# Kernel optimization log

Hardware: AMD Instinct MI355X
Metric: run time of the kernel (lower is better)

## Reference

```python
import jax, jax.numpy as jnp
import numpy as np

B, S, D = 2, 2048, 4096
H, KVH, HD = 32, 8, 128
WIN = 1024  # sliding window
THETA = 10000.0


def setup_inputs() -> dict:
    key = jax.random.key(0)
    ks = jax.random.split(key, 5)
    x = jax.random.normal(ks[0], (B, S, D), jnp.float32) * 0.02
    wq = jax.random.normal(ks[1], (H * HD, D), jnp.float32) * 0.02
    wk = jax.random.normal(ks[2], (KVH * HD, D), jnp.float32) * 0.02
    wv = jax.random.normal(ks[3], (KVH * HD, D), jnp.float32) * 0.02
    wo = jax.random.normal(ks[4], (D, H * HD), jnp.float32) * 0.02
    positions = jnp.arange(S, dtype=jnp.int32)
    inv_freq = 1.0 / (THETA ** (jnp.arange(0, HD, 2, dtype=jnp.float32) / HD))
    ang = positions.astype(jnp.float32)[:, None] * inv_freq[None, :]  # [S, HD/2]
    cos, sin = jnp.cos(ang), jnp.sin(ang)
    i = jnp.arange(S)[:, None]
    j = jnp.arange(S)[None, :]
    allowed = (j <= i) & (i - j < WIN)  # causal + sliding window
    mask = jnp.where(allowed, 0.0, -1e9).astype(jnp.float32)  # [S, S]
    return {"x": x, "wq": wq, "wk": wk, "wv": wv, "wo": wo,
            "cos": cos, "sin": sin, "mask": mask, "positions": positions}


def _apply_rope(t, cos, sin):
    # t: [B, S, nH, HD]; pairs are consecutive dims (torch view_as_complex layout)
    tr = t.reshape(t.shape[:-1] + (HD // 2, 2))
    t0, t1 = tr[..., 0], tr[..., 1]
    c = cos[None, :, None, :]
    s = sin[None, :, None, :]
    out = jnp.stack([t0 * c - t1 * s, t0 * s + t1 * c], axis=-1)
    return out.reshape(t.shape)


def reference(x, wq, wk, wv, wo, cos, sin, mask, positions):
    bsz, seqlen, _ = x.shape
    xq = (x @ wq.T).reshape(bsz, seqlen, H, HD)
    xk = (x @ wk.T).reshape(bsz, seqlen, KVH, HD)
    xv = (x @ wv.T).reshape(bsz, seqlen, KVH, HD)
    xq = _apply_rope(xq, cos, sin)
    xk = _apply_rope(xk, cos, sin)
    # GQA: repeat_kv head broadcast (prefill path: positions.size(0) > 1)
    rep = H // KVH
    key = jnp.repeat(xk, rep, axis=2)  # [B, S, H, HD]
    val = jnp.repeat(xv, rep, axis=2)
    q = xq.transpose(0, 2, 1, 3)  # [B, H, S, HD]
    k = key.transpose(0, 2, 1, 3)
    v = val.transpose(0, 2, 1, 3)
    scale = HD ** -0.5
    scores = jnp.einsum("bhqd,bhkd->bhqk", q, k) * scale
    scores = scores + mask[None, None, :, :]
    probs = jax.nn.softmax(scores.astype(jnp.float32), axis=-1).astype(q.dtype)
    out = jnp.einsum("bhqk,bhkd->bhqd", probs, v)
    out = out.transpose(0, 2, 1, 3).reshape(bsz, seqlen, H * HD)
    return out @ wo.T
```

## Files before the change

kernel.cpp:

```cpp
#include <hip/hip_runtime.h>
#include <hip/hip_bf16.h>

#define B_  2
#define S_  2048
#define D_  4096
#define H_  32
#define KVH_ 8
#define HD_ 128
#define WIN_ 1024
#define KVSTR 2048

typedef __attribute__((ext_vector_type(8))) __bf16 bf16x8;
typedef __attribute__((ext_vector_type(4))) float f32x4;
using bf16 = __hip_bfloat16;

typedef const __attribute__((address_space(1))) void* gas_ptr;
typedef __attribute__((address_space(3))) void* las_ptr;

__device__ __forceinline__ void gload16(const void* g, void* l) {
    __builtin_amdgcn_global_load_lds((gas_ptr)g, (las_ptr)l, 16, 0, 0);
}

__device__ __forceinline__ bf16x8 load8(const bf16* p) {
    return *reinterpret_cast<const bf16x8*>(p);
}
__device__ __forceinline__ bf16x8 cvt8(const bf16* p) {
    return *reinterpret_cast<const bf16x8*>(p);
}
__device__ __forceinline__ bf16x8 cvt8(const float* p) {
    const float4* q = reinterpret_cast<const float4*>(p);
    float4 a = q[0], b = q[1];
    bf16x8 r;
    r[0] = (__bf16)a.x; r[1] = (__bf16)a.y; r[2] = (__bf16)a.z; r[3] = (__bf16)a.w;
    r[4] = (__bf16)b.x; r[5] = (__bf16)b.y; r[6] = (__bf16)b.z; r[7] = (__bf16)b.w;
    return r;
}
__device__ __forceinline__ void store1(float* p, float v) { *p = v; }
__device__ __forceinline__ void store1(bf16* p, float v) { *p = __float2bfloat16(v); }

#define GBAR()  __builtin_amdgcn_s_barrier()
#define SCB0()  __builtin_amdgcn_sched_barrier(0)
#define LGKM0() do { asm volatile("s_waitcnt lgkmcnt(0)" ::: "memory"); \
                     __builtin_amdgcn_sched_barrier(0); } while (0)
#define VMC(n)  do { asm volatile("s_waitcnt vmcnt(" #n ")" ::: "memory"); \
                     __builtin_amdgcn_sched_barrier(0); } while (0)

__global__ __launch_bounds__(256) void cast_kernel(const float* __restrict__ in,
                                                   bf16* __restrict__ out) {
    long i = ((long)blockIdx.x * 256 + threadIdx.x) * 8;
    const float4* p = reinterpret_cast<const float4*>(in + i);
    float4 a = p[0], b = p[1];
    bf16x8 r;
    r[0] = (__bf16)a.x; r[1] = (__bf16)a.y; r[2] = (__bf16)a.z; r[3] = (__bf16)a.w;
    r[4] = (__bf16)b.x; r[5] = (__bf16)b.y; r[6] = (__bf16)b.z; r[7] = (__bf16)b.w;
    *reinterpret_cast<bf16x8*>(out + i) = r;
}

__global__ __launch_bounds__(256) void cast2_kernel(
    const float* __restrict__ in0, bf16* __restrict__ out0,
    const float* __restrict__ in1, bf16* __restrict__ out1, int n0blocks) {
    const bool first = (int)blockIdx.x < n0blocks;
    const float* in = first ? in0 : in1;
    bf16* out = first ? out0 : out1;
    long bid = first ? blockIdx.x : (blockIdx.x - n0blocks);
    long i = (bid * 256 + threadIdx.x) * 8;
    const float4* p = reinterpret_cast<const float4*>(in + i);
    float4 a = p[0], b = p[1];
    bf16x8 r;
    r[0] = (__bf16)a.x; r[1] = (__bf16)a.y; r[2] = (__bf16)a.z; r[3] = (__bf16)a.w;
    r[4] = (__bf16)b.x; r[5] = (__bf16)b.y; r[6] = (__bf16)b.z; r[7] = (__bf16)b.w;
    *reinterpret_cast<bf16x8*>(out + i) = r;
}

__device__ __forceinline__ void xcd_swizzle(int& bx, int& by, int nbx, int nby) {
    int flat = bx + nbx * by;
    int nwg  = nbx * nby;
    int cpx  = nwg >> 3;
    int swz  = (flat & 7) * cpx + (flat >> 3);
    bx = swz % nbx;
    by = swz / nbx;
}

template <typename TC>
__global__ __launch_bounds__(512, 2) void gemm_nt_256(
    const bf16* __restrict__ A, const bf16* __restrict__ Bm,
    TC* __restrict__ C, int M, int N, int K) {
    __shared__ __bf16 lds[2][2][256 * 64];

    const int tid  = threadIdx.x;
    const int wave = tid >> 6;
    const int lane = tid & 63;
    const int col  = lane & 15;
    const int quad = lane >> 4;
    const int c7   = col & 7;
    const int wmi  = wave >> 2;
    const int wni  = wave & 3;
    int bx = blockIdx.x, by = blockIdx.y;
    xcd_swizzle(bx, by, gridDim.x, gridDim.y);
    const long m0  = (long)by * 256;
    const long n0  = (long)bx * 256;
    const int  nt  = K >> 6;

    f32x4 zero = {0.f, 0.f, 0.f, 0.f};
    f32x4 acc[8][4];
#pragma unroll
    for (int i = 0; i < 8; i++)
#pragma unroll
        for (int j = 0; j < 4; j++) acc[i][j] = zero;

    long gA[4], gB[4];
    int  lofs[4];
#pragma unroll
    for (int j = 0; j < 4; j++) {
        int r  = j * 64 + wave * 8 + (lane >> 3);
        int cg = (lane & 7) ^ (r & 7);
        gA[j]   = (m0 + r) * (long)K + cg * 8;
        gB[j]   = (n0 + r) * (long)K + cg * 8;
        lofs[j] = (j * 64 + wave * 8) * 128;
    }

#pragma unroll
    for (int j = 0; j < 4; j++) {
        gload16(A  + gA[j], (char*)lds[0][0] + lofs[j]);
        gload16(Bm + gB[j], (char*)lds[0][1] + lofs[j]);
    }
    if (nt > 1) {
#pragma unroll
        for (int j = 0; j < 4; j++)
            gload16(Bm + gB[j] + 64, (char*)lds[1][1] + lofs[j]);
        gload16(A + gA[0] + 64, (char*)lds[1][0] + lofs[0]);
        gload16(A + gA[2] + 64, (char*)lds[1][0] + lofs[2]);
        VMC(6);
    } else {
        VMC(0);
    }
    GBAR();

#define RDA_(dst, mf, ks) \
    dst = *reinterpret_cast<const bf16x8*>(Ab + (wmi * 128 + (mf) * 16 + col) * 128 \
                                              + ((((ks) << 2) + quad) ^ c7) * 16)
#define MFMA16(mb) \
    do { \
        _Pragma("unroll") \
        for (int ks = 0; ks < 2; ks++) { \
            _Pragma("unroll") \
            for (int nf = 0; nf < 4; nf++) { \
                acc[mb][nf]     = __builtin_amdgcn_mfma_f32_16x16x32_bf16( \
                    a[0][ks], bfr[nf][ks], acc[mb][nf], 0, 0, 0); \
                acc[mb + 1][nf] = __builtin_amdgcn_mfma_f32_16x16x32_bf16( \
                    a[1][ks], bfr[nf][ks], acc[mb + 1][nf], 0, 0, 0); \
            } \
        } \
    } while (0)

    for (int t = 0; t < nt; ++t) {
        const int cur = t & 1;
        const char* Ab = (const char*)lds[cur][0];
        const char* Bb = (const char*)lds[cur][1];
        char* An2 = (char*)lds[cur ^ 1][0];
        char* Ac2 = (char*)lds[cur][0];
        char* Bc2 = (char*)lds[cur][1];

        bf16x8 bfr[4][2];
#pragma unroll
        for (int nf = 0; nf < 4; nf++)
#pragma unroll
            for (int ks = 0; ks < 2; ks++)
                bfr[nf][ks] = *reinterpret_cast<const bf16x8*>(
                    Bb + (wni * 64 + nf * 16 + col) * 128 + (((ks << 2) + quad) ^ c7) * 16);
        bf16x8 a[2][2];
        RDA_(a[0][0], 0, 0); RDA_(a[0][1], 0, 1);
        RDA_(a[1][0], 1, 0); RDA_(a[1][1], 1, 1);
        if (t + 1 < nt) {
            long ko = (long)(t + 1) * 64;
            gload16(A + gA[1] + ko, An2 + lofs[1]);
            gload16(A + gA[3] + ko, An2 + lofs[3]);
        }
        GBAR();
        LGKM0();
        __builtin_amdgcn_s_setprio(1);
        MFMA16(0);
        __builtin_amdgcn_s_setprio(0);
        GBAR();

        RDA_(a[0][0], 2, 0); RDA_(a[0][1], 2, 1);
        RDA_(a[1][0], 3, 0); RDA_(a[1][1], 3, 1);
        if (t + 2 < nt) {
            long ko = (long)(t + 2) * 64;
#pragma unroll
            for (int j = 0; j < 4; j++)
                gload16(Bm + gB[j] + ko, Bc2 + lofs[j]);
        }
        GBAR();
        LGKM0();
        __builtin_amdgcn_s_setprio(1);
        MFMA16(2);
        __builtin_amdgcn_s_setprio(0);
        GBAR();

        RDA_(a[0][0], 4, 0); RDA_(a[0][1], 4, 1);
        RDA_(a[1][0], 5, 0); RDA_(a[1][1], 5, 1);
        if (t + 2 < nt) {
            long ko = (long)(t + 2) * 64;
            gload16(A + gA[0] + ko, Ac2 + lofs[0]);
            gload16(A + gA[2] + ko, Ac2 + lofs[2]);
        }
        GBAR();
        LGKM0();
        __builtin_amdgcn_s_setprio(1);
        MFMA16(4);
        __builtin_amdgcn_s_setprio(0);
        GBAR();

        RDA_(a[0][0], 6, 0); RDA_(a[0][1], 6, 1);
        RDA_(a[1][0], 7, 0); RDA_(a[1][1], 7, 1);
        LGKM0();
        __builtin_amdgcn_s_setprio(1);
        MFMA16(6);
        __builtin_amdgcn_s_setprio(0);
        if (t + 2 < nt) { VMC(6); } else { VMC(0); }
        GBAR();
    }

#pragma unroll
    for (int mf = 0; mf < 8; mf++) {
#pragma unroll
        for (int nf = 0; nf < 4; nf++) {
            long row = m0 + wmi * 128 + mf * 16 + quad * 4;
            long cc  = n0 + wni * 64 + nf * 16 + col;
#pragma unroll
            for (int r = 0; r < 4; r++)
                store1(&C[(row + r) * (long)N + cc], acc[mf][nf][r]);
        }
    }
}

template <typename TC>
__global__ __launch_bounds__(256) void gemm_nt_fast(
    const bf16* __restrict__ A, const bf16* __restrict__ Bm,
    TC* __restrict__ C, int M, int N, int K) {
    __shared__ __bf16 As[128 * 64];
    __shared__ __bf16 Bs[128 * 64];

    const int tid  = threadIdx.x;
    const int wave = tid >> 6;
    const int lane = tid & 63;
    const int col  = lane & 15;
    const int quad = lane >> 4;
    const int c7   = col & 7;
    const int wm   = (wave >> 1) * 64;
    const int wn   = (wave & 1) * 64;
    int bx = blockIdx.x, by = blockIdx.y;
    xcd_swizzle(bx, by, gridDim.x, gridDim.y);
    const long m0  = (long)by * 128;
    const long n0  = (long)bx * 128;

    f32x4 zero = {0.f, 0.f, 0.f, 0.f};
    f32x4 acc[4][4];
#pragma unroll
    for (int i = 0; i < 4; i++)
#pragma unroll
        for (int j = 0; j < 4; j++) acc[i][j] = zero;

    long goffA[4], goffB[4];
    int  loff[4];
#pragma unroll
    for (int i = 0; i < 4; i++) {
        int r  = (wave * 4 + i) * 8 + (lane >> 3);
        int cg = (lane & 7) ^ (r & 7);
        goffA[i] = (m0 + r) * (long)K + cg * 8;
        goffB[i] = (n0 + r) * (long)K + cg * 8;
        loff[i]  = (wave * 4 + i) * 1024;
    }

    for (int kt = 0; kt < K; kt += 64) {
#pragma unroll
        for (int i = 0; i < 4; i++) {
            gload16(A + goffA[i] + kt, (char*)As + loff[i]);
            gload16(Bm + goffB[i] + kt, (char*)Bs + loff[i]);
        }
        __syncthreads();

        bf16x8 af[2][4], bfv[2][4];
#pragma unroll
        for (int ks = 0; ks < 2; ks++) {
#pragma unroll
            for (int mt = 0; mt < 4; mt++) {
                int row = wm + mt * 16 + col;
                af[ks][mt] = *reinterpret_cast<const bf16x8*>(
                    (const char*)As + row * 128 + (((ks << 2) + quad) ^ c7) * 16);
            }
#pragma unroll
            for (int nt = 0; nt < 4; nt++) {
                int row = wn + nt * 16 + col;
                bfv[ks][nt] = *reinterpret_cast<const bf16x8*>(
                    (const char*)Bs + row * 128 + (((ks << 2) + quad) ^ c7) * 16);
            }
        }
#pragma unroll
        for (int ks = 0; ks < 2; ks++)
#pragma unroll
            for (int mt = 0; mt < 4; mt++)
#pragma unroll
                for (int nt = 0; nt < 4; nt++)
                    acc[mt][nt] = __builtin_amdgcn_mfma_f32_16x16x32_bf16(
                        af[ks][mt], bfv[ks][nt], acc[mt][nt], 0, 0, 0);
        __syncthreads();
    }

#pragma unroll
    for (int mt = 0; mt < 4; mt++) {
#pragma unroll
        for (int nt = 0; nt < 4; nt++) {
            long row = m0 + wm + mt * 16 + quad * 4;
            long cc  = n0 + wn + nt * 16 + col;
#pragma unroll
            for (int r = 0; r < 4; r++)
                store1(&C[(row + r) * (long)N + cc], acc[mt][nt][r]);
        }
    }
}

template <typename TA, typename TB, typename TC>
__global__ __launch_bounds__(256) void gemm_nt(
    const TA* __restrict__ A, const TB* __restrict__ Bm,
    TC* __restrict__ C, int M, int N, int K, int ldc) {
    __shared__ __bf16 As[128 * 40];
    __shared__ __bf16 Bs[128 * 40];

    const int tid  = threadIdx.x;
    const int wave = tid >> 6;
    const int lane = tid & 63;
    const int col  = lane & 15;
    const int quad = lane >> 4;
    const int wm   = (wave >> 1) * 64;
    const int wn   = (wave & 1) * 64;
    const long m0  = (long)blockIdx.y * 128;
    const long n0  = (long)blockIdx.x * 128;

    f32x4 zero = {0.f, 0.f, 0.f, 0.f};
    f32x4 acc[4][4];
#pragma unroll
    for (int i = 0; i < 4; i++)
#pragma unroll
        for (int j = 0; j < 4; j++) acc[i][j] = zero;

    const int srow = tid >> 2;
    const int sch  = (tid & 3) * 8;

    for (int kt = 0; kt < K; kt += 32) {
        bf16x8 av0 = cvt8(A + (m0 + srow)      * (long)K + kt + sch);
        bf16x8 av1 = cvt8(A + (m0 + srow + 64) * (long)K + kt + sch);
        bf16x8 bv0 = cvt8(Bm + (n0 + srow)      * (long)K + kt + sch);
        bf16x8 bv1 = cvt8(Bm + (n0 + srow + 64) * (long)K + kt + sch);
        *reinterpret_cast<bf16x8*>(&As[srow * 40 + sch])        = av0;
        *reinterpret_cast<bf16x8*>(&As[(srow + 64) * 40 + sch]) = av1;
        *reinterpret_cast<bf16x8*>(&Bs[srow * 40 + sch])        = bv0;
        *reinterpret_cast<bf16x8*>(&Bs[(srow + 64) * 40 + sch]) = bv1;
        __syncthreads();

        bf16x8 af[4], bfv[4];
#pragma unroll
        for (int mt = 0; mt < 4; mt++)
            af[mt] = *reinterpret_cast<const bf16x8*>(&As[(wm + mt * 16 + col) * 40 + quad * 8]);
#pragma unroll
        for (int nt = 0; nt < 4; nt++)
            bfv[nt] = *reinterpret_cast<const bf16x8*>(&Bs[(wn + nt * 16 + col) * 40 + quad * 8]);
#pragma unroll
        for (int mt = 0; mt < 4; mt++)
#pragma unroll
            for (int nt = 0; nt < 4; nt++)
                acc[mt][nt] = __builtin_amdgcn_mfma_f32_16x16x32_bf16(
                    af[mt], bfv[nt], acc[mt][nt], 0, 0, 0);
        __syncthreads();
    }

#pragma unroll
    for (int mt = 0; mt < 4; mt++) {
#pragma unroll
        for (int nt = 0; nt < 4; nt++) {
            long row = m0 + wm + mt * 16 + quad * 4;
            long cc  = n0 + wn + nt * 16 + col;
#pragma unroll
            for (int r = 0; r < 4; r++)
                store1(&C[(row + r) * (long)ldc + cc], acc[mt][nt][r]);
        }
    }
}

__global__ __launch_bounds__(256) void rope_kv_kernel(
    bf16* __restrict__ kvb,
    const float* __restrict__ cosb, const float* __restrict__ sinb) {
    int idx = blockIdx.x * 256 + threadIdx.x;
    int pair = idx & 63;
    int rest = idx >> 6;
    int hh   = rest % KVH_;
    int tok  = rest / KVH_;
    int s    = tok & (S_ - 1);
    long base = (long)tok * KVSTR + hh * HD_ + pair * 2;
    float c  = cosb[s * 64 + pair];
    float sn = sinb[s * 64 + pair];
    float t0 = __bfloat162float(kvb[base]);
    float t1 = __bfloat162float(kvb[base + 1]);
    kvb[base]     = __float2bfloat16(t0 * c - t1 * sn);
    kvb[base + 1] = __float2bfloat16(t0 * sn + t1 * c);
}

__global__ __launch_bounds__(256) void transpose_v(const bf16* __restrict__ kv,
                                                   bf16* __restrict__ vt) {
    __shared__ __bf16 tile[64][72];
    const int s0 = blockIdx.x * 64;
    const int d0 = blockIdx.y * 64;
    const int b  = blockIdx.z;
    const int tid = threadIdx.x;
    const int tr  = tid >> 3;
    const int c8  = (tid & 7) * 8;
#pragma unroll
    for (int p = 0; p < 2; p++) {
        int srow = tr + p * 32;
        bf16x8 val = load8(kv + ((long)(b * S_ + s0 + srow)) * KVSTR + 1024 + d0 + c8);
        *reinterpret_cast<bf16x8*>(&tile[srow][c8]) = val;
    }
    __syncthreads();
#pragma unroll
    for (int p = 0; p < 2; p++) {
        int dd = tr + p * 32;
        bf16x8 ov;
#pragma unroll
        for (int j = 0; j < 8; j++) ov[j] = tile[c8 + j][dd];
        *reinterpret_cast<bf16x8*>(vt + ((long)(b * 1024 + d0 + dd)) * S_ + s0 + c8) = ov;
    }
}

__global__ __launch_bounds__(512, 4) void attn_kernel(
    const bf16* __restrict__ q, const bf16* __restrict__ kv,
    const bf16* __restrict__ vt, bf16* __restrict__ o,
    const float* __restrict__ cosb, const float* __restrict__ sinb) {
    const int qb  = blockIdx.x;
    const int hp  = blockIdx.y;
    const int b   = blockIdx.z;
    const int tid = threadIdx.x;
    const int wave = tid >> 6;
    const int lane = tid & 63;
    const int col  = lane & 15;
    const int quad = lane >> 4;
    const int h    = hp * 2 + (wave >> 2);
    const int wq4  = wave & 3;
    const int kvh  = hp >> 1;
    const int i0   = qb * 64;
    const float scale = 0.08838834764831845f;

    __shared__ __bf16 Ks[64 * 128];
    __shared__ __bf16 Vs[128 * 64];
    __shared__ __bf16 Pl[8][16 * 72];

    const int srow = i0 + wq4 * 16 + col;
    bf16x8 qa[4];
    {
        const bf16* qptr = q + ((long)(b * S_ + srow)) * (H_ * HD_) + h * HD_ + quad * 8;
#pragma unroll
        for (int ks = 0; ks < 4; ks++) {
            bf16x8 v = load8(qptr + ks * 32);
            float4 c4 = *reinterpret_cast<const float4*>(
                cosb + (long)srow * 64 + quad * 4 + ks * 16);
            float4 s4 = *reinterpret_cast<const float4*>(
                sinb + (long)srow * 64 + quad * 4 + ks * 16);
            bf16x8 r;
            float t0, t1;
            t0 = (float)v[0]; t1 = (float)v[1];
            r[0] = (__bf16)(t0 * c4.x - t1 * s4.x); r[1] = (__bf16)(t0 * s4.x + t1 * c4.x);
            t0 = (float)v[2]; t1 = (float)v[3];
            r[2] = (__bf16)(t0 * c4.y - t1 * s4.y); r[3] = (__bf16)(t0 * s4.y + t1 * c4.y);
            t0 = (float)v[4]; t1 = (float)v[5];
            r[4] = (__bf16)(t0 * c4.z - t1 * s4.z); r[5] = (__bf16)(t0 * s4.z + t1 * c4.z);
            t0 = (float)v[6]; t1 = (float)v[7];
            r[6] = (__bf16)(t0 * c4.w - t1 * s4.w); r[7] = (__bf16)(t0 * s4.w + t1 * c4.w);
            qa[ks] = r;
        }
    }

    long gK[2], gV[2];
    int  lK[2], lV[2];
#pragma unroll
    for (int i = 0; i < 2; i++) {
        int ck  = wave * 2 + i;
        int rK  = ck * 4 + (lane >> 4);
        int cgK = (lane & 15) ^ (rK & 15);
        gK[i] = ((long)(b * S_) + rK) * KVSTR + kvh * HD_ + cgK * 8;
        lK[i] = ck * 1024;
        int rV  = ck * 8 + (lane >> 3);
        int cgV = (lane & 7) ^ (rV & 7);
        gV[i] = ((long)(b * 1024) + kvh * HD_ + rV) * (long)S_ + cgV * 8;
        lV[i] = ck * 1024;
    }

    f32x4 zero = {0.f, 0.f, 0.f, 0.f};
    f32x4 oacc[8];
#pragma unroll
    for (int i = 0; i < 8; i++) oacc[i] = zero;
    float lsum[4] = {0.f, 0.f, 0.f, 0.f};

    const int kb0 = (qb >= 16) ? (qb - 16) : 0;

    bf16x8 kreg[2], vreg[2];
#pragma unroll
    for (int i = 0; i < 2; i++) {
        kreg[i] = *reinterpret_cast<const bf16x8*>(kv + gK[i] + (long)kb0 * 64 * KVSTR);
        vreg[i] = *reinterpret_cast<const bf16x8*>(vt + gV[i] + kb0 * 64);
    }

    for (int kb = kb0; kb <= qb; kb++) {
        GBAR();
        SCB0();
#pragma unroll
        for (int i = 0; i < 2; i++) {
            *reinterpret_cast<bf16x8*>((char*)Ks + lK[i] + lane * 16) = kreg[i];
            *reinterpret_cast<bf16x8*>((char*)Vs + lV[i] + lane * 16) = vreg[i];
        }
        LGKM0();
        GBAR();
        SCB0();
        if (kb < qb) {
#pragma unroll
            for (int i = 0; i < 2; i++) {
                kreg[i] = *reinterpret_cast<const bf16x8*>(
                    kv + gK[i] + (long)(kb + 1) * 64 * KVSTR);
                vreg[i] = *reinterpret_cast<const bf16x8*>(
                    vt + gV[i] + (kb + 1) * 64);
            }
            SCB0();
        }

        f32x4 sfr[4];
        __builtin_amdgcn_s_setprio(1);
#pragma unroll
        for (int nt = 0; nt < 4; nt++) {
            f32x4 s = zero;
            int row = nt * 16 + col;
#pragma unroll
            for (int ks = 0; ks < 4; ks++) {
                bf16x8 bfv = *reinterpret_cast<const bf16x8*>(
                    (const char*)Ks + row * 256 + (((ks << 2) + quad) ^ col) * 16);
                s = __builtin_amdgcn_mfma_f32_16x16x32_bf16(qa[ks], bfv, s, 0, 0, 0);
            }
            sfr[nt] = s;
        }
        __builtin_amdgcn_s_setprio(0);
#pragma unroll
        for (int nt = 0; nt < 4; nt++) {
            int j = kb * 64 + nt * 16 + col;
#pragma unroll
            for (int r = 0; r < 4; r++) {
                int i = i0 + wq4 * 16 + quad * 4 + r;
                float p = 0.f;
                if (j <= i && (i - j) < WIN_) p = __expf(sfr[nt][r] * scale);
                lsum[r] += p;
                Pl[wave][(quad * 4 + r) * 72 + nt * 16 + col] = __float2bfloat16(p);
            }
        }
        __builtin_amdgcn_s_setprio(1);
#pragma unroll
        for (int ks2 = 0; ks2 < 2; ks2++) {
            bf16x8 pa = *reinterpret_cast<const bf16x8*>(
                &Pl[wave][col * 72 + ks2 * 32 + quad * 8]);
#pragma unroll
            for (int nt2 = 0; nt2 < 8; nt2++) {
                int d = nt2 * 16 + col;
                bf16x8 vb = *reinterpret_cast<const bf16x8*>(
                    (const char*)Vs + d * 128 + ((((ks2 << 2) + quad)) ^ (col & 7)) * 16);
                oacc[nt2] = __builtin_amdgcn_mfma_f32_16x16x32_bf16(
                    pa, vb, oacc[nt2], 0, 0, 0);
            }
        }
        __builtin_amdgcn_s_setprio(0);
    }

#pragma unroll
    for (int m = 1; m < 16; m <<= 1) {
#pragma unroll
        for (int r = 0; r < 4; r++) lsum[r] += __shfl_xor(lsum[r], m, 64);
    }

    bf16* op = o + ((long)(b * S_ + i0 + wq4 * 16 + quad * 4)) * (H_ * HD_) + h * HD_;
#pragma unroll
    for (int nt2 = 0; nt2 < 8; nt2++) {
#pragma unroll
        for (int r = 0; r < 4; r++)
            op[(long)r * (H_ * HD_) + nt2 * 16 + col] =
                __float2bfloat16(oacc[nt2][r] / lsum[r]);
    }
}

extern "C" void kernel_launch(void* const* d_in, const int* in_sizes, int n_in,
                              void* d_out, int out_size, void* d_ws, size_t ws_size,
                              hipStream_t stream) {
    const float* x    = (const float*)d_in[0];
    const float* wq   = (const float*)d_in[1];
    const float* wk   = (const float*)d_in[2];
    const float* wv   = (const float*)d_in[3];
    const float* wo   = (const float*)d_in[4];
    const float* cosb = (const float*)d_in[5];
    const float* sinb = (const float*)d_in[6];
    float* out = (float*)d_out;

    const size_t T   = (size_t)B_ * S_;
    const size_t SZ_D  = T * (H_ * HD_);
    const size_t SZ_KV = T * (KVH_ * HD_);

    dim3 blk(256);
    const size_t need_fast = (SZ_D * 3 + SZ_KV * 3 + SZ_D) * 2;

    if (ws_size >= need_fast) {
        bf16* xb    = (bf16*)d_ws;
        bf16* wbuf  = xb    + SZ_D;
        bf16* q_ws  = wbuf  + SZ_D;
        bf16* kv_ws = q_ws  + SZ_D;
        bf16* vt_ws = kv_ws + 2 * SZ_KV;
        bf16* ao_ws = vt_ws + SZ_KV;

        cast2_kernel<<<2 * (SZ_D / 2048), blk, 0, stream>>>(x, xb, wq, wbuf,
                                                            (int)(SZ_D / 2048));
        gemm_nt_256<bf16><<<dim3(16, 16), dim3(512), 0, stream>>>(xb, wbuf, q_ws, 4096, 4096, 4096);

        cast2_kernel<<<2 * (SZ_KV / 2048), blk, 0, stream>>>(wk, wbuf, wv, wbuf + SZ_KV,
                                                             (int)(SZ_KV / 2048));
        gemm_nt_fast<bf16><<<dim3(16, 32), blk, 0, stream>>>(xb, wbuf, kv_ws, 4096, 2048, 4096);

        rope_kv_kernel<<<(B_ * S_ * KVH_ * 64) / 256, blk, 0, stream>>>(
            kv_ws, cosb, sinb);
        transpose_v<<<dim3(32, 16, 2), blk, 0, stream>>>(kv_ws, vt_ws);

        attn_kernel<<<dim3(32, 16, 2), dim3(512), 0, stream>>>(
            q_ws, kv_ws, vt_ws, ao_ws, cosb, sinb);

        cast_kernel<<<SZ_D / 2048, blk, 0, stream>>>(wo, wbuf);
        gemm_nt_256<float><<<dim3(16, 16), dim3(512), 0, stream>>>(ao_ws, wbuf, out, 4096, 4096, 4096);
    } else {
        bf16* q_ws  = (bf16*)d_ws;
        bf16* kv_ws = q_ws  + SZ_D;
        bf16* vt_ws = kv_ws + 2 * SZ_KV;
        bf16* ao_ws = vt_ws + SZ_KV;

        gemm_nt<float, float, bf16><<<dim3(32, 32), blk, 0, stream>>>(x, wq, q_ws, 4096, 4096, 4096, 4096);
        gemm_nt<float, float, bf16><<<dim3(8, 32),  blk, 0, stream>>>(x, wk, kv_ws, 4096, 1024, 4096, KVSTR);
        gemm_nt<float, float, bf16><<<dim3(8, 32),  blk, 0, stream>>>(x, wv, kv_ws + 1024, 4096, 1024, 4096, KVSTR);

        rope_kv_kernel<<<(B_ * S_ * KVH_ * 64) / 256, blk, 0, stream>>>(
            kv_ws, cosb, sinb);
        transpose_v<<<dim3(32, 16, 2), blk, 0, stream>>>(kv_ws, vt_ws);

        attn_kernel<<<dim3(32, 16, 2), dim3(512), 0, stream>>>(
            q_ws, kv_ws, vt_ws, ao_ws, cosb, sinb);

        gemm_nt<bf16, float, float><<<dim3(32, 32), blk, 0, stream>>>(ao_ws, wo, out, 4096, 4096, 4096, 4096);
    }
}
```

Before: 660.2 us.

## Fuse Q, K, V projections into one GEMM over a concatenated weight matrix

Concatenates wq, wk and wv into one bf16 weight buffer and runs a single 256-tile GEMM that writes an interleaved QKV buffer with row stride 6144. The RoPE, V-transpose and attention kernels are re-pointed at offsets inside that buffer. This removes the separate smaller KV GEMM and its tail, so the 384-block launch fills the GPU better. The attention output now reuses the x cast buffer to save workspace. The wider row stride can change cache and locality behaviour for the K loads in attention.

Result: slower. 707.5 us (+7.2%).

```diff
diff --git a/kernel.cpp b/kernel.cpp
--- a/kernel.cpp
+++ b/kernel.cpp
@@ -8,7 +8,9 @@
 #define KVH_ 8
 #define HD_ 128
 #define WIN_ 1024
-#define KVSTR 2048
+#define QKVSTR 6144
+#define KOFF   4096
+#define VOFF   5120
 
 typedef __attribute__((ext_vector_type(8))) __bf16 bf16x8;
 typedef __attribute__((ext_vector_type(4))) float f32x4;
@@ -235,92 +237,6 @@
     }
 }
 
-template <typename TC>
-__global__ __launch_bounds__(256) void gemm_nt_fast(
-    const bf16* __restrict__ A, const bf16* __restrict__ Bm,
-    TC* __restrict__ C, int M, int N, int K) {
-    __shared__ __bf16 As[128 * 64];
-    __shared__ __bf16 Bs[128 * 64];
-
-    const int tid  = threadIdx.x;
-    const int wave = tid >> 6;
-    const int lane = tid & 63;
-    const int col  = lane & 15;
-    const int quad = lane >> 4;
-    const int c7   = col & 7;
-    const int wm   = (wave >> 1) * 64;
-    const int wn   = (wave & 1) * 64;
-    int bx = blockIdx.x, by = blockIdx.y;
-    xcd_swizzle(bx, by, gridDim.x, gridDim.y);
-    const long m0  = (long)by * 128;
-    const long n0  = (long)bx * 128;
-
-    f32x4 zero = {0.f, 0.f, 0.f, 0.f};
-    f32x4 acc[4][4];
-#pragma unroll
-    for (int i = 0; i < 4; i++)
-#pragma unroll
-        for (int j = 0; j < 4; j++) acc[i][j] = zero;
-
-    long goffA[4], goffB[4];
-    int  loff[4];
-#pragma unroll
-    for (int i = 0; i < 4; i++) {
-        int r  = (wave * 4 + i) * 8 + (lane >> 3);
-        int cg = (lane & 7) ^ (r & 7);
-        goffA[i] = (m0 + r) * (long)K + cg * 8;
-        goffB[i] = (n0 + r) * (long)K + cg * 8;
-        loff[i]  = (wave * 4 + i) * 1024;
-    }
-
-    for (int kt = 0; kt < K; kt += 64) {
-#pragma unroll
-        for (int i = 0; i < 4; i++) {
-            gload16(A + goffA[i] + kt, (char*)As + loff[i]);
-            gload16(Bm + goffB[i] + kt, (char*)Bs + loff[i]);
-        }
-        __syncthreads();
-
-        bf16x8 af[2][4], bfv[2][4];
-#pragma unroll
-        for (int ks = 0; ks < 2; ks++) {
-#pragma unroll
-            for (int mt = 0; mt < 4; mt++) {
-                int row = wm + mt * 16 + col;
-                af[ks][mt] = *reinterpret_cast<const bf16x8*>(
-                    (const char*)As + row * 128 + (((ks << 2) + quad) ^ c7) * 16);
-            }
-#pragma unroll
-            for (int nt = 0; nt < 4; nt++) {
-                int row = wn + nt * 16 + col;
-                bfv[ks][nt] = *reinterpret_cast<const bf16x8*>(
-                    (const char*)Bs + row * 128 + (((ks << 2) + quad) ^ c7) * 16);
-            }
-        }
-#pragma unroll
-        for (int ks = 0; ks < 2; ks++)
-#pragma unroll
-            for (int mt = 0; mt < 4; mt++)
-#pragma unroll
-                for (int nt = 0; nt < 4; nt++)
-                    acc[mt][nt] = __builtin_amdgcn_mfma_f32_16x16x32_bf16(
-                        af[ks][mt], bfv[ks][nt], acc[mt][nt], 0, 0, 0);
-        __syncthreads();
-    }
-
-#pragma unroll
-    for (int mt = 0; mt < 4; mt++) {
-#pragma unroll
-        for (int nt = 0; nt < 4; nt++) {
-            long row = m0 + wm + mt * 16 + quad * 4;
-            long cc  = n0 + wn + nt * 16 + col;
-#pragma unroll
-            for (int r = 0; r < 4; r++)
-                store1(&C[(row + r) * (long)N + cc], acc[mt][nt][r]);
-        }
-    }
-}
-
 template <typename TA, typename TB, typename TC>
 __global__ __launch_bounds__(256) void gemm_nt(
     const TA* __restrict__ A, const TB* __restrict__ Bm,
@@ -389,7 +305,7 @@
 }
 
 __global__ __launch_bounds__(256) void rope_kv_kernel(
-    bf16* __restrict__ kvb,
+    bf16* __restrict__ qkv,
     const float* __restrict__ cosb, const float* __restrict__ sinb) {
     int idx = blockIdx.x * 256 + threadIdx.x;
     int pair = idx & 63;
@@ -397,16 +313,16 @@
     int hh   = rest % KVH_;
     int tok  = rest / KVH_;
     int s    = tok & (S_ - 1);
-    long base = (long)tok * KVSTR + hh * HD_ + pair * 2;
+    long base = (long)tok * QKVSTR + KOFF + hh * HD_ + pair * 2;
     float c  = cosb[s * 64 + pair];
     float sn = sinb[s * 64 + pair];
-    float t0 = __bfloat162float(kvb[base]);
-    float t1 = __bfloat162float(kvb[base + 1]);
-    kvb[base]     = __float2bfloat16(t0 * c - t1 * sn);
-    kvb[base + 1] = __float2bfloat16(t0 * sn + t1 * c);
-}
-
-__global__ __launch_bounds__(256) void transpose_v(const bf16* __restrict__ kv,
+    float t0 = __bfloat162float(qkv[base]);
+    float t1 = __bfloat162float(qkv[base + 1]);
+    qkv[base]     = __float2bfloat16(t0 * c - t1 * sn);
+    qkv[base + 1] = __float2bfloat16(t0 * sn + t1 * c);
+}
+
+__global__ __launch_bounds__(256) void transpose_v(const bf16* __restrict__ qkv,
                                                    bf16* __restrict__ vt) {
     __shared__ __bf16 tile[64][72];
     const int s0 = blockIdx.x * 64;
@@ -418,7 +334,7 @@
 #pragma unroll
     for (int p = 0; p < 2; p++) {
         int srow = tr + p * 32;
-        bf16x8 val = load8(kv + ((long)(b * S_ + s0 + srow)) * KVSTR + 1024 + d0 + c8);
+        bf16x8 val = load8(qkv + ((long)(b * S_ + s0 + srow)) * QKVSTR + VOFF + d0 + c8);
         *reinterpret_cast<bf16x8*>(&tile[srow][c8]) = val;
     }
     __syncthreads();
@@ -433,8 +349,8 @@
 }
 
 __global__ __launch_bounds__(512, 4) void attn_kernel(
-    const bf16* __restrict__ q, const bf16* __restrict__ kv,
-    const bf16* __restrict__ vt, bf16* __restrict__ o,
+    const bf16* __restrict__ qkv, const bf16* __restrict__ vt,
+    bf16* __restrict__ o,
     const float* __restrict__ cosb, const float* __restrict__ sinb) {
     const int qb  = blockIdx.x;
     const int hp  = blockIdx.y;
@@ -457,7 +373,7 @@
     const int srow = i0 + wq4 * 16 + col;
     bf16x8 qa[4];
     {
-        const bf16* qptr = q + ((long)(b * S_ + srow)) * (H_ * HD_) + h * HD_ + quad * 8;
+        const bf16* qptr = qkv + ((long)(b * S_ + srow)) * QKVSTR + h * HD_ + quad * 8;
 #pragma unroll
         for (int ks = 0; ks < 4; ks++) {
             bf16x8 v = load8(qptr + ks * 32);
@@ -486,7 +402,7 @@
         int ck  = wave * 2 + i;
         int rK  = ck * 4 + (lane >> 4);
         int cgK = (lane & 15) ^ (rK & 15);
-        gK[i] = ((long)(b * S_) + rK) * KVSTR + kvh * HD_ + cgK * 8;
+        gK[i] = ((long)(b * S_) + rK) * QKVSTR + KOFF + kvh * HD_ + cgK * 8;
         lK[i] = ck * 1024;
         int rV  = ck * 8 + (lane >> 3);
         int cgV = (lane & 7) ^ (rV & 7);
@@ -505,7 +421,7 @@
     bf16x8 kreg[2], vreg[2];
 #pragma unroll
     for (int i = 0; i < 2; i++) {
-        kreg[i] = *reinterpret_cast<const bf16x8*>(kv + gK[i] + (long)kb0 * 64 * KVSTR);
+        kreg[i] = *reinterpret_cast<const bf16x8*>(qkv + gK[i] + (long)kb0 * 64 * QKVSTR);
         vreg[i] = *reinterpret_cast<const bf16x8*>(vt + gV[i] + kb0 * 64);
     }
 
@@ -524,7 +440,7 @@
 #pragma unroll
             for (int i = 0; i < 2; i++) {
                 kreg[i] = *reinterpret_cast<const bf16x8*>(
-                    kv + gK[i] + (long)(kb + 1) * 64 * KVSTR);
+                    qkv + gK[i] + (long)(kb + 1) * 64 * QKVSTR);
                 vreg[i] = *reinterpret_cast<const bf16x8*>(
                     vt + gV[i] + (kb + 1) * 64);
             }
@@ -603,55 +519,60 @@
     const float* sinb = (const float*)d_in[6];
     float* out = (float*)d_out;
 
-    const size_t T   = (size_t)B_ * S_;
-    const size_t SZ_D  = T * (H_ * HD_);
-    const size_t SZ_KV = T * (KVH_ * HD_);
+    const size_t T      = (size_t)B_ * S_;
+    const size_t SZ_D   = T * (H_ * HD_);
+    const size_t SZ_KV  = T * (KVH_ * HD_);
+    const size_t SZ_QKV = T * QKVSTR;
+    const size_t SZ_WQKV = (size_t)QKVSTR * D_;
 
     dim3 blk(256);
-    const size_t need_fast = (SZ_D * 3 + SZ_KV * 3 + SZ_D) * 2;
+    const size_t need_fast = (SZ_D + SZ_WQKV + SZ_QKV + SZ_KV) * 2;
 
     if (ws_size >= need_fast) {
         bf16* xb    = (bf16*)d_ws;
-        bf16* wbuf  = xb    + SZ_D;
-        bf16* q_ws  = wbuf  + SZ_D;
-        bf16* kv_ws = q_ws  + SZ_D;
-        bf16* vt_ws = kv_ws + 2 * SZ_KV;
+        bf16* wqkv  = xb    + SZ_D;
+        bf16* qkv   = wqkv  + SZ_WQKV;
+        bf16* vt_ws = qkv   + SZ_QKV;
+        bf16* ao_ws = xb;
+
+        cast2_kernel<<<(int)((SZ_D + SZ_D) / 2048), blk, 0, stream>>>(
+            x, xb, wq, wqkv, (int)(SZ_D / 2048));
+        cast2_kernel<<<(int)((SZ_KV + SZ_KV) / 2048), blk, 0, stream>>>(
+            wk, wqkv + SZ_D, wv, wqkv + SZ_D + SZ_KV, (int)(SZ_KV / 2048));
+
+        gemm_nt_256<bf16><<<dim3(24, 16), dim3(512), 0, stream>>>(
+            xb, wqkv, qkv, 4096, QKVSTR, 4096);
+
+        rope_kv_kernel<<<(B_ * S_ * KVH_ * 64) / 256, blk, 0, stream>>>(
+            qkv, cosb, sinb);
+        transpose_v<<<dim3(32, 16, 2), blk, 0, stream>>>(qkv, vt_ws);
+
+        attn_kernel<<<dim3(32, 16, 2), dim3(512), 0, stream>>>(
+            qkv, vt_ws, ao_ws, cosb, sinb);
+
+        cast_kernel<<<SZ_D / 2048, blk, 0, stream>>>(wo, wqkv);
+        gemm_nt_256<float><<<dim3(16, 16), dim3(512), 0, stream>>>(
+            ao_ws, wqkv, out, 4096, 4096, 4096);
+    } else {
+        bf16* qkv   = (bf16*)d_ws;
+        bf16* vt_ws = qkv + SZ_QKV;
         bf16* ao_ws = vt_ws + SZ_KV;
 
-        cast2_kernel<<<2 * (SZ_D / 2048), blk, 0, stream>>>(x, xb, wq, wbuf,
-                                                            (int)(SZ_D / 2048));
-        gemm_nt_256<bf16><<<dim3(16, 16), dim3(512), 0, stream>>>(xb, wbuf, q_ws, 4096, 4096, 4096);
-
-        cast2_kernel<<<2 * (SZ_KV / 2048), blk, 0, stream>>>(wk, wbuf, wv, wbuf + SZ_KV,
-                                                             (int)(SZ_KV / 2048));
-        gemm_nt_fast<bf16><<<dim3(16, 32), blk, 0, stream>>>(xb, wbuf, kv_ws, 4096, 2048, 4096);
+        gemm_nt<float, float, bf16><<<dim3(32, 32), blk, 0, stream>>>(
+            x, wq, qkv, 4096, 4096, 4096, QKVSTR);
+        gemm_nt<float, float, bf16><<<dim3(8, 32),  blk, 0, stream>>>(
+            x, wk, qkv + KOFF, 4096, 1024, 4096, QKVSTR);
+        gemm_nt<float, float, bf16><<<dim3(8, 32),  blk, 0, stream>>>(
+            x, wv, qkv + VOFF, 4096, 1024, 4096, QKVSTR);
 
         rope_kv_kernel<<<(B_ * S_ * KVH_ * 64) / 256, blk, 0, stream>>>(
-            kv_ws, cosb, sinb);
-        transpose_v<<<dim3(32, 16, 2), blk, 0, stream>>>(kv_ws, vt_ws);
+            qkv, cosb, sinb);
+        transpose_v<<<dim3(32, 16, 2), blk, 0, stream>>>(qkv, vt_ws);
 
         attn_kernel<<<dim3(32, 16, 2), dim3(512), 0, stream>>>(
-            q_ws, kv_ws, vt_ws, ao_ws, cosb, sinb);
-
-        cast_kernel<<<SZ_D / 2048, blk, 0, stream>>>(wo, wbuf);
-        gemm_nt_256<float><<<dim3(16, 16), dim3(512), 0, stream>>>(ao_ws, wbuf, out, 4096, 4096, 4096);
-    } else {
-        bf16* q_ws  = (bf16*)d_ws;
-        bf16* kv_ws = q_ws  + SZ_D;
-        bf16* vt_ws = kv_ws + 2 * SZ_KV;
-        bf16* ao_ws = vt_ws + SZ_KV;
-
-        gemm_nt<float, float, bf16><<<dim3(32, 32), blk, 0, stream>>>(x, wq, q_ws, 4096, 4096, 4096, 4096);
-        gemm_nt<float, float, bf16><<<dim3(8, 32),  blk, 0, stream>>>(x, wk, kv_ws, 4096, 1024, 4096, KVSTR);
-        gemm_nt<float, float, bf16><<<dim3(8, 32),  blk, 0, stream>>>(x, wv, kv_ws + 1024, 4096, 1024, 4096, KVSTR);
-
-        rope_kv_kernel<<<(B_ * S_ * KVH_ * 64) / 256, blk, 0, stream>>>(
-            kv_ws, cosb, sinb);
-        transpose_v<<<dim3(32, 16, 2), blk, 0, stream>>>(kv_ws, vt_ws);
-
-        attn_kernel<<<dim3(32, 16, 2), dim3(512), 0, stream>>>(
-            q_ws, kv_ws, vt_ws, ao_ws, cosb, sinb);
-
-        gemm_nt<bf16, float, float><<<dim3(32, 32), blk, 0, stream>>>(ao_ws, wo, out, 4096, 4096, 4096, 4096);
-    }
-}
+            qkv, vt_ws, ao_ws, cosb, sinb);
+
+        gemm_nt<bf16, float, float><<<dim3(32, 32), blk, 0, stream>>>(
+            ao_ws, wo, out, 4096, 4096, 4096, 4096);
+    }
+}
```
